# Kernel tuning notes

Hardware: AMD Instinct MI355X
Metric: run time of the kernel (lower is better)

## Reference

```python
import jax, jax.numpy as jnp
import numpy as np

INPUT_SIZE = 512
HIDDEN_SIZE = 512
BATCH = 32
SEQ = 2048
NUM_LAYERS = 1


def setup_inputs() -> dict:
    key = jax.random.key(0)
    k_in, k_wih, k_whh, k_bih, k_bhh = jax.random.split(key, 5)
    std = 1.0 / (HIDDEN_SIZE ** 0.5)
    inp = {
        "input": jax.random.normal(k_in, (BATCH, SEQ, INPUT_SIZE), dtype=jnp.float32),
        "h0": jnp.zeros((NUM_LAYERS, BATCH, HIDDEN_SIZE), dtype=jnp.float32),
        "weight_ih": jax.random.uniform(k_wih, (3 * HIDDEN_SIZE, INPUT_SIZE), minval=-std, maxval=std, dtype=jnp.float32),
        "weight_hh": jax.random.uniform(k_whh, (3 * HIDDEN_SIZE, HIDDEN_SIZE), minval=-std, maxval=std, dtype=jnp.float32),
        "bias_ih": jax.random.uniform(k_bih, (3 * HIDDEN_SIZE,), minval=-std, maxval=std, dtype=jnp.float32),
        "bias_hh": jax.random.uniform(k_bhh, (3 * HIDDEN_SIZE,), minval=-std, maxval=std, dtype=jnp.float32),
    }
    return inp


def reference(input, h0, weight_ih, weight_hh, bias_ih, bias_hh):
    # Standard GRU recurrence (dequantized math of the custom CUDA quantized GRU).
    # input: [B, T, I] (batch_first), h0: [1, B, H]
    # Precompute input-side gates in one big GEMM: [B, T, 3H] -> [T, B, 3H]
    x_gates = jnp.einsum("bti,gi->btg", input, weight_ih) + bias_ih
    x_gates = jnp.swapaxes(x_gates, 0, 1)

    def step(h, xg):
        hg = h @ weight_hh.T + bias_hh  # [B, 3H]
        xr, xz, xn = jnp.split(xg, 3, axis=-1)
        hr, hz, hn = jnp.split(hg, 3, axis=-1)
        r = jax.nn.sigmoid(xr + hr)
        z = jax.nn.sigmoid(xz + hz)
        n = jnp.tanh(xn + r * hn)
        h_new = (1.0 - z) * n + z * h
        return h_new, h_new

    _, hs = jax.lax.scan(step, h0[0], x_gates)  # hs: [T, B, H]
    return jnp.swapaxes(hs, 0, 1)  # [B, T, H]
```

## Files before the change

kernel.cpp:

```cpp
#include <hip/hip_runtime.h>


#define T_SEQ 2048
#define BATCH 32
#define ISZ 512
#define HSZ 512
#define NG 32
#define CW 16
#define KP 520
#define XF 520
#define SLOTS 4
#define TAGB 0x80000000u

typedef short bf16x8 __attribute__((ext_vector_type(8)));
typedef float f32x4 __attribute__((ext_vector_type(4)));

__device__ __forceinline__ unsigned short f2bf(float f) {
  unsigned int u = __float_as_uint(f);
  unsigned int r = u + 0x7FFFu + ((u >> 16) & 1u);
  return (unsigned short)(r >> 16);
}

__device__ __forceinline__ void gl2lds16(const float* gsrc, void* lds) {
  __builtin_amdgcn_global_load_lds(
      (const __attribute__((address_space(1))) void*)gsrc,
      (__attribute__((address_space(3))) void*)lds, 16, 0, 0);
}

__device__ __forceinline__ void stage_plain(const float* base, long rowStride,
                                            unsigned short (*Bst)[KP], int tid) {
  if (tid < 256) {
    const int b = tid >> 3, part = tid & 7;
    const float* src = base + (long)b * rowStride;
#pragma unroll
    for (int i = 0; i < 16; ++i) {
      const int c16 = i * 8 + part;
      const float4 f = *(const float4*)(src + c16 * 4);
      ushort4 u;
      u.x = f2bf(f.x); u.y = f2bf(f.y); u.z = f2bf(f.z); u.w = f2bf(f.w);
      *(ushort4*)(&Bst[b][c16 * 4]) = u;
    }
  }
}

__device__ __forceinline__ void stage_hx(const unsigned long long* slot,
                                         const unsigned int want,
                                         unsigned short (*Bst)[KP], int tid) {
  if (tid < 256) {
    const int b = tid >> 3, part = tid & 7;
    const unsigned long long* src = slot + (long)b * (HSZ / 2) + part;
    unsigned long long tmp[32];
#pragma unroll
    for (int i = 0; i < 32; ++i)
      tmp[i] = __hip_atomic_load(src + i * 8, __ATOMIC_RELAXED,
                                 __HIP_MEMORY_SCOPE_AGENT);
    for (;;) {
      unsigned int bad = 0;
#pragma unroll
      for (int i = 0; i < 32; ++i)
        bad |= ((unsigned int)(tmp[i] >> 32)) ^ want;
      if (bad == 0) break;
#pragma unroll
      for (int i = 0; i < 32; ++i)
        tmp[i] = __hip_atomic_load(src + i * 8, __ATOMIC_RELAXED,
                                   __HIP_MEMORY_SCOPE_AGENT);
    }
#pragma unroll
    for (int i = 0; i < 32; ++i) {
      const int c = i * 8 + part;
      *(unsigned int*)(&Bst[b][c * 2]) = (unsigned int)tmp[i];
    }
  }
}

__device__ __forceinline__ f32x4 mfma_slab(const bf16x8* a,
                                           unsigned short (*Bst)[KP],
                                           int bt, int n16, int quad) {
  f32x4 acc = {0.f, 0.f, 0.f, 0.f};
#pragma unroll
  for (int kk = 0; kk < 16; ++kk) {
    const bf16x8 bf = *(const bf16x8*)(&Bst[bt * 16 + n16][kk * 32 + quad * 8]);
    acc = __builtin_amdgcn_mfma_f32_16x16x32_bf16(a[kk], bf, acc, 0, 0, 0);
  }
  return acc;
}

__global__ __launch_bounds__(384, 1) void gru_persistent(
    const float* __restrict__ in, const float* __restrict__ h0,
    const float* __restrict__ wih, const float* __restrict__ whh,
    const float* __restrict__ bihp, const float* __restrict__ bhhp,
    float* __restrict__ out, unsigned long long* __restrict__ hx) {
  __shared__ unsigned short Bh[BATCH][KP];
  __shared__ unsigned short Bx[BATCH][KP];
  __shared__ float Bxf[BATCH][XF];
  __shared__ float xg[3][CW][33];
  __shared__ float hg[3][CW][33];
  __shared__ float own_h[CW][33];
  __shared__ float bih_l[48], bhh_l[48];

  const int tid = threadIdx.x;
  const int g = blockIdx.x;
  const int c0 = g * CW;
  const int lane = tid & 63, wid = tid >> 6;
  const int n16 = lane & 15, quad = lane >> 4;
  const int rt = wid % 3, bt = wid / 3;
  const int sb = tid >> 3, sp = tid & 7;

  if (tid < 48) bih_l[tid] = bihp[(tid >> 4) * HSZ + c0 + (tid & 15)];
  else if (tid >= 64 && tid < 112) {
    const int lr = tid - 64;
    bhh_l[lr] = bhhp[(lr >> 4) * HSZ + c0 + (lr & 15)];
  }

  if (tid < 256) {
#pragma unroll
    for (int s = 0; s < SLOTS; ++s)
      __hip_atomic_store(hx + (long)s * BATCH * (HSZ / 2) + sb * (HSZ / 2) + g * 8 + sp,
                         0ULL, __ATOMIC_RELAXED, __HIP_MEMORY_SCOPE_AGENT);
  }

  bf16x8 a_hh[16], a_ih[16];
  {
    const long grow = rt * HSZ + c0 + n16;
    const float* wr_h = whh + grow * HSZ;
    const float* wr_i = wih + grow * ISZ;
#pragma unroll
    for (int kk = 0; kk < 16; ++kk) {
      const int k0 = kk * 32 + quad * 8;
      float4 f0 = *(const float4*)(wr_h + k0);
      float4 f1 = *(const float4*)(wr_h + k0 + 4);
      bf16x8 v;
      v[0] = (short)f2bf(f0.x); v[1] = (short)f2bf(f0.y);
      v[2] = (short)f2bf(f0.z); v[3] = (short)f2bf(f0.w);
      v[4] = (short)f2bf(f1.x); v[5] = (short)f2bf(f1.y);
      v[6] = (short)f2bf(f1.z); v[7] = (short)f2bf(f1.w);
      a_hh[kk] = v;
      f0 = *(const float4*)(wr_i + k0);
      f1 = *(const float4*)(wr_i + k0 + 4);
      v[0] = (short)f2bf(f0.x); v[1] = (short)f2bf(f0.y);
      v[2] = (short)f2bf(f0.z); v[3] = (short)f2bf(f0.w);
      v[4] = (short)f2bf(f1.x); v[5] = (short)f2bf(f1.y);
      v[6] = (short)f2bf(f1.z); v[7] = (short)f2bf(f1.w);
      a_ih[kk] = v;
    }
  }
  asm volatile("s_waitcnt vmcnt(0)" ::: "memory");

  stage_plain(in, (long)T_SEQ * ISZ, Bx, tid);
  __syncthreads();
  {
    f32x4 acc = mfma_slab(a_ih, Bx, bt, n16, quad);
#pragma unroll
    for (int r = 0; r < 4; ++r)
      xg[rt][quad * 4 + r][bt * 16 + n16] = acc[r] + bih_l[rt * 16 + quad * 4 + r];
  }
  __syncthreads();

  for (int t = 0; t < T_SEQ; ++t) {
    if (t + 1 < T_SEQ) {
      const float* tb = in + (long)(t + 1) * ISZ + (lane << 2);
#pragma unroll
      for (int b = wid; b < BATCH; b += 6) {
        const float* src = tb + (long)b * T_SEQ * ISZ;
        gl2lds16(src, &Bxf[b][0]);
        gl2lds16(src + 256, &Bxf[b][256]);
      }
    }

    if (t == 0) {
      stage_plain(h0, HSZ, Bh, tid);
      if (tid < 256) {
        own_h[2 * sp][sb] = h0[sb * HSZ + c0 + 2 * sp];
        own_h[2 * sp + 1][sb] = h0[sb * HSZ + c0 + 2 * sp + 1];
      }
    } else {
      stage_hx(hx + (long)((t - 1) & (SLOTS - 1)) * BATCH * (HSZ / 2),
               TAGB + (unsigned)(t - 1), Bh, tid);
    }
    asm volatile("s_waitcnt vmcnt(0)" ::: "memory");
    __syncthreads();

    {
      f32x4 acc = mfma_slab(a_hh, Bh, bt, n16, quad);
#pragma unroll
      for (int r = 0; r < 4; ++r)
        hg[rt][quad * 4 + r][bt * 16 + n16] = acc[r];
    }
    if (t + 1 < T_SEQ && tid < 256) {
#pragma unroll
      for (int i = 0; i < 16; ++i) {
        const int c16 = i * 8 + sp;
        const float4 f = *(const float4*)(&Bxf[sb][c16 * 4]);
        ushort4 u;
        u.x = f2bf(f.x); u.y = f2bf(f.y); u.z = f2bf(f.z); u.w = f2bf(f.w);
        *(ushort4*)(&Bx[sb][c16 * 4]) = u;
      }
    }
    __syncthreads();

    if (tid < 256) {
      float h2[2];
#pragma unroll
      for (int jj = 0; jj < 2; ++jj) {
        const int col = 2 * sp + jj;
        const float xr = xg[0][col][sb], xz = xg[1][col][sb], xn = xg[2][col][sb];
        const float hr = hg[0][col][sb] + bhh_l[col];
        const float hz = hg[1][col][sb] + bhh_l[16 + col];
        const float hn = hg[2][col][sb] + bhh_l[32 + col];
        const float r = 1.f / (1.f + __expf(-(xr + hr)));
        const float z = 1.f / (1.f + __expf(-(xz + hz)));
        const float aa = xn + r * hn;
        const float e = __expf(-2.f * fabsf(aa));
        float th = (1.f - e) / (1.f + e);
        th = copysignf(th, aa);
        const float hp = own_h[col][sb];
        const float hnew = (1.f - z) * th + z * hp;
        own_h[col][sb] = hnew;
        h2[jj] = hnew;
      }
      const unsigned int lo =
          (unsigned int)f2bf(h2[0]) | ((unsigned int)f2bf(h2[1]) << 16);
      const unsigned long long val =
          ((unsigned long long)(TAGB + (unsigned)t) << 32) | lo;
      __hip_atomic_store(hx + (long)(t & (SLOTS - 1)) * BATCH * (HSZ / 2) +
                             sb * (HSZ / 2) + g * 8 + sp,
                         val, __ATOMIC_RELAXED, __HIP_MEMORY_SCOPE_AGENT);
      const unsigned long long o2 =
          ((unsigned long long)__float_as_uint(h2[1]) << 32) |
          (unsigned long long)__float_as_uint(h2[0]);
      __builtin_nontemporal_store(
          o2, (unsigned long long*)(out + (long)sb * T_SEQ * HSZ +
                                    (long)t * HSZ + c0 + 2 * sp));
    }
    __syncthreads();

    if (t + 1 < T_SEQ) {
      f32x4 acc = mfma_slab(a_ih, Bx, bt, n16, quad);
#pragma unroll
      for (int r = 0; r < 4; ++r)
        xg[rt][quad * 4 + r][bt * 16 + n16] =
            acc[r] + bih_l[rt * 16 + quad * 4 + r];
      __syncthreads();
    }
  }
}

extern "C" void kernel_launch(void* const* d_in, const int* in_sizes, int n_in,
                              void* d_out, int out_size, void* d_ws, size_t ws_size,
                              hipStream_t stream) {
  const float* in  = (const float*)d_in[0];
  const float* h0  = (const float*)d_in[1];
  const float* wih = (const float*)d_in[2];
  const float* whh = (const float*)d_in[3];
  const float* bih = (const float*)d_in[4];
  const float* bhh = (const float*)d_in[5];
  float* out = (float*)d_out;
  unsigned long long* hx = (unsigned long long*)d_ws;

  gru_persistent<<<dim3(NG), dim3(384), 0, stream>>>(in, h0, wih, whh, bih, bhh,
                                                     out, hx);
}
```

Measured before the change: 14.27 ms.

## Co-locate persistent GRU blocks on one XCD and use local-scope flag polling

The kernel now launches 256 blocks. Each block reads its XCC id, and the first XCD to claim a control word keeps 32 blocks that take group ids atomically while all other blocks exit. Because every participating block then shares the same L2, hidden-state exchange stores use workgroup scope and the polling loads use inline asm with sc0 instead of agent-scope atomics. This is meant to cut cross-XCD coherence latency on the per-timestep spin barrier. The slot count drops to 2, and a memset of the control area is added each call. Relying on L2 coherence within one XCD with weaker scopes is fragile.

Result: faster. 13.04 ms (-8.6%).

```diff
diff --git a/kernel.cpp b/kernel.cpp
--- a/kernel.cpp
+++ b/kernel.cpp
@@ -9,8 +9,9 @@
 #define CW 16
 #define KP 520
 #define XF 520
-#define SLOTS 4
+#define SLOTS 2
 #define TAGB 0x80000000u
+#define CTL_BYTES 4096
 
 typedef short bf16x8 __attribute__((ext_vector_type(8)));
 typedef float f32x4 __attribute__((ext_vector_type(4)));
@@ -43,27 +44,38 @@
   }
 }
 
+__device__ __forceinline__ void issue32(unsigned long long* tmp, unsigned voff,
+                                        const unsigned long long* base) {
+#define LD1(i)                                                        \
+  asm volatile("global_load_dwordx2 %0, %1, %2 offset:%3 sc0"         \
+               : "=v"(tmp[i])                                         \
+               : "v"(voff), "s"(base), "i"((i) * 64));
+  LD1(0)  LD1(1)  LD1(2)  LD1(3)  LD1(4)  LD1(5)  LD1(6)  LD1(7)
+  LD1(8)  LD1(9)  LD1(10) LD1(11) LD1(12) LD1(13) LD1(14) LD1(15)
+  LD1(16) LD1(17) LD1(18) LD1(19) LD1(20) LD1(21) LD1(22) LD1(23)
+  LD1(24) LD1(25) LD1(26) LD1(27) LD1(28) LD1(29) LD1(30) LD1(31)
+#undef LD1
+}
+
 __device__ __forceinline__ void stage_hx(const unsigned long long* slot,
                                          const unsigned int want,
                                          unsigned short (*Bst)[KP], int tid) {
   if (tid < 256) {
     const int b = tid >> 3, part = tid & 7;
-    const unsigned long long* src = slot + (long)b * (HSZ / 2) + part;
+    const unsigned voff = (unsigned)((b * (HSZ / 2) + part) * 8);
     unsigned long long tmp[32];
-#pragma unroll
-    for (int i = 0; i < 32; ++i)
-      tmp[i] = __hip_atomic_load(src + i * 8, __ATOMIC_RELAXED,
-                                 __HIP_MEMORY_SCOPE_AGENT);
+    issue32(tmp, voff, slot);
     for (;;) {
+      asm volatile("s_waitcnt vmcnt(0)" ::: "memory");
+      __builtin_amdgcn_sched_barrier(0);
+#pragma unroll
+      for (int i = 0; i < 32; ++i) asm volatile("" : "+v"(tmp[i]));
       unsigned int bad = 0;
 #pragma unroll
       for (int i = 0; i < 32; ++i)
         bad |= ((unsigned int)(tmp[i] >> 32)) ^ want;
       if (bad == 0) break;
-#pragma unroll
-      for (int i = 0; i < 32; ++i)
-        tmp[i] = __hip_atomic_load(src + i * 8, __ATOMIC_RELAXED,
-                                   __HIP_MEMORY_SCOPE_AGENT);
+      issue32(tmp, voff, slot);
     }
 #pragma unroll
     for (int i = 0; i < 32; ++i) {
@@ -89,7 +101,8 @@
     const float* __restrict__ in, const float* __restrict__ h0,
     const float* __restrict__ wih, const float* __restrict__ whh,
     const float* __restrict__ bihp, const float* __restrict__ bhhp,
-    float* __restrict__ out, unsigned long long* __restrict__ hx) {
+    float* __restrict__ out, unsigned int* __restrict__ ctl,
+    unsigned long long* __restrict__ hx) {
   __shared__ unsigned short Bh[BATCH][KP];
   __shared__ unsigned short Bx[BATCH][KP];
   __shared__ float Bxf[BATCH][XF];
@@ -97,9 +110,29 @@
   __shared__ float hg[3][CW][33];
   __shared__ float own_h[CW][33];
   __shared__ float bih_l[48], bhh_l[48];
+  __shared__ int s_ok, s_g;
 
   const int tid = threadIdx.x;
-  const int g = blockIdx.x;
+
+  const unsigned xcc = __builtin_amdgcn_s_getreg(63508) & 0xFu;
+  if (tid == 0) {
+    unsigned expected = 0u;
+    __hip_atomic_compare_exchange_strong(&ctl[0], &expected, xcc + 1u,
+                                         __ATOMIC_RELAXED, __ATOMIC_RELAXED,
+                                         __HIP_MEMORY_SCOPE_AGENT);
+    const unsigned tgt = (expected == 0u) ? (xcc + 1u) : expected;
+    int ok = (tgt == xcc + 1u);
+    int gg = 0;
+    if (ok)
+      gg = (int)__hip_atomic_fetch_add(&ctl[1], 1u, __ATOMIC_RELAXED,
+                                       __HIP_MEMORY_SCOPE_AGENT);
+    s_ok = ok && (gg < NG);
+    s_g = gg;
+  }
+  __syncthreads();
+  if (!s_ok) return;
+  const int g = s_g;
+
   const int c0 = g * CW;
   const int lane = tid & 63, wid = tid >> 6;
   const int n16 = lane & 15, quad = lane >> 4;
@@ -116,7 +149,7 @@
 #pragma unroll
     for (int s = 0; s < SLOTS; ++s)
       __hip_atomic_store(hx + (long)s * BATCH * (HSZ / 2) + sb * (HSZ / 2) + g * 8 + sp,
-                         0ULL, __ATOMIC_RELAXED, __HIP_MEMORY_SCOPE_AGENT);
+                         0ULL, __ATOMIC_RELAXED, __HIP_MEMORY_SCOPE_WORKGROUP);
   }
 
   bf16x8 a_hh[16], a_ih[16];
@@ -224,7 +257,7 @@
           ((unsigned long long)(TAGB + (unsigned)t) << 32) | lo;
       __hip_atomic_store(hx + (long)(t & (SLOTS - 1)) * BATCH * (HSZ / 2) +
                              sb * (HSZ / 2) + g * 8 + sp,
-                         val, __ATOMIC_RELAXED, __HIP_MEMORY_SCOPE_AGENT);
+                         val, __ATOMIC_RELAXED, __HIP_MEMORY_SCOPE_WORKGROUP);
       const unsigned long long o2 =
           ((unsigned long long)__float_as_uint(h2[1]) << 32) |
           (unsigned long long)__float_as_uint(h2[0]);
@@ -255,8 +288,12 @@
   const float* bih = (const float*)d_in[4];
   const float* bhh = (const float*)d_in[5];
   float* out = (float*)d_out;
-  unsigned long long* hx = (unsigned long long*)d_ws;
-
-  gru_persistent<<<dim3(NG), dim3(384), 0, stream>>>(in, h0, wih, whh, bih, bhh,
-                                                     out, hx);
-}
+  unsigned int* ctl = (unsigned int*)d_ws;
+  unsigned long long* hx =
+      (unsigned long long*)((char*)d_ws + CTL_BYTES);
+
+  hipMemsetAsync(d_ws, 0, CTL_BYTES, stream);
+
+  gru_persistent<<<dim3(256), dim3(384), 0, stream>>>(in, h0, wih, whh, bih,
+                                                      bhh, out, ctl, hx);
+}
```
